# Performance work log

Hardware: AMD Instinct MI355X
Metric: run time of the kernel (lower is better)

Reference implementation:

```python
import jax, jax.numpy as jnp
import numpy as np

T = 8192   # sequence length (timesteps)
C = 1      # input channels
H = 51     # hidden size (module default)


def setup_inputs() -> dict:
    key = jax.random.key(0)
    ks = jax.random.split(key, 12)
    s = 1.0 / np.sqrt(H)  # PyTorch LSTMCell/Linear uniform init bound

    def u(k, shape):
        return jax.random.uniform(k, shape, jnp.float32, -s, s)

    return {
        "x": jax.random.normal(ks[0], (T, C), jnp.float32),
        # LSTMCell 1: input C -> hidden H
        "Wih1": u(ks[1], (4 * H, C)),
        "Whh1": u(ks[2], (4 * H, H)),
        "bih1": u(ks[3], (4 * H,)),
        "bhh1": u(ks[4], (4 * H,)),
        # LSTMCell 2: hidden H -> hidden H
        "Wih2": u(ks[5], (4 * H, H)),
        "Whh2": u(ks[6], (4 * H, H)),
        "bih2": u(ks[7], (4 * H,)),
        "bhh2": u(ks[8], (4 * H,)),
        # Output linear: H -> 1
        "Wlin": u(ks[9], (1, H)),
        "blin": u(ks[10], (1,)),
    }


def _lstm_cell(xt, h, c, Wih, Whh, bih, bhh):
    # PyTorch LSTMCell gate order: i, f, g, o
    z = xt @ Wih.T + h @ Whh.T + (bih + bhh)  # [1, 4H]
    i, f, g, o = jnp.split(z, 4, axis=-1)
    c_new = jax.nn.sigmoid(f) * c + jax.nn.sigmoid(i) * jnp.tanh(g)
    h_new = jax.nn.sigmoid(o) * jnp.tanh(c_new)
    return h_new, c_new


def reference(x, Wih1, Whh1, bih1, bhh1, Wih2, Whh2, bih2, bhh2, Wlin, blin):
    def step(carry, xt):
        h1, c1, h2, c2 = carry
        h1, c1 = _lstm_cell(xt, h1, c1, Wih1, Whh1, bih1, bhh1)
        h2, c2 = _lstm_cell(h1, h2, c2, Wih2, Whh2, bih2, bhh2)
        out = h2 @ Wlin.T + blin  # [1, 1]
        return (h1, c1, h2, c2), out[0]

    init = tuple(jnp.zeros((1, H), jnp.float32) for _ in range(4))
    _, outs = jax.lax.scan(step, init, x[:, None, :])  # per-step xt: [1, C]
    return outs  # [T, 1]
```

## Files before the change

kernel.cpp:

```cpp
#include <hip/hip_runtime.h>

#define TSTEPS 8192
#define H 51
#define SE 8
#define NEPOCH (TSTEPS / SE + 3)

typedef float  f2 __attribute__((ext_vector_type(2)));
typedef float  f4 __attribute__((ext_vector_type(4)));
typedef int    i4 __attribute__((ext_vector_type(4)));
typedef int    i2 __attribute__((ext_vector_type(2)));
typedef _Float16 h2 __attribute__((ext_vector_type(2)));

__device__ __forceinline__ int rl_i(int v, int k) { return __builtin_amdgcn_readlane(v, k); }
__device__ __forceinline__ h2 asp(int v) { union { int i; h2 h; } u; u.i = v; return u.h; }
__device__ __forceinline__ int ash(h2 v) { union { int i; h2 h; } u; u.h = v; return u.i; }

__device__ __forceinline__ float fdot2(h2 a, h2 b, float c) {
#if __has_builtin(__builtin_amdgcn_fdot2)
    return __builtin_amdgcn_fdot2(a, b, c, false);
#else
    return fmaf((float)a[0], (float)b[0], fmaf((float)a[1], (float)b[1], c));
#endif
}
__device__ __forceinline__ float sigmoidf_fast(float x) {
    return __builtin_amdgcn_rcpf(1.0f + __expf(-x));
}
__device__ __forceinline__ float tanhf_fast(float x) {
    x = fminf(fmaxf(x, -15.0f), 15.0f);
    float t = __expf(-2.0f * x);
    return (1.0f - t) * __builtin_amdgcn_rcpf(1.0f + t);
}
__device__ __forceinline__ int packpair(const float* Wrow, int j) {
    const float w0 = (2 * j < H) ? Wrow[2 * j] : 0.0f;
    const float w1 = (2 * j + 1 < H) ? Wrow[2 * j + 1] : 0.0f;
    h2 p; p[0] = (_Float16)w0; p[1] = (_Float16)w1; return ash(p);
}
__device__ __forceinline__ int packpairs_bperm(float hval, int a0, int a1) {
    const int hi = __float_as_int(hval);
    const float v0 = __int_as_float(__builtin_amdgcn_ds_bpermute(a0, hi));
    const float v1 = __int_as_float(__builtin_amdgcn_ds_bpermute(a1, hi));
    h2 pk; pk[0] = (_Float16)v0; pk[1] = (_Float16)v1;
    return ash(pk);
}

#define DECLG(g) i4 wq##g##_0, wq##g##_1, wq##g##_2, wq##g##_3, wq##g##_4, wq##g##_5; i2 wq##g##_6;
#define LOADG(g, RP) { const float* _r = (RP); \
    i4 t0 = {packpair(_r,0),  packpair(_r,1),  packpair(_r,2),  packpair(_r,3)};  wq##g##_0 = t0; \
    i4 t1 = {packpair(_r,4),  packpair(_r,5),  packpair(_r,6),  packpair(_r,7)};  wq##g##_1 = t1; \
    i4 t2 = {packpair(_r,8),  packpair(_r,9),  packpair(_r,10), packpair(_r,11)}; wq##g##_2 = t2; \
    i4 t3 = {packpair(_r,12), packpair(_r,13), packpair(_r,14), packpair(_r,15)}; wq##g##_3 = t3; \
    i4 t4 = {packpair(_r,16), packpair(_r,17), packpair(_r,18), packpair(_r,19)}; wq##g##_4 = t4; \
    i4 t5 = {packpair(_r,20), packpair(_r,21), packpair(_r,22), packpair(_r,23)}; wq##g##_5 = t5; \
    i2 t6 = {packpair(_r,24), packpair(_r,25)};                                   wq##g##_6 = t6; }
#define PING(g) asm("" : "+v"(wq##g##_0), "+v"(wq##g##_1), "+v"(wq##g##_2), \
                        "+v"(wq##g##_3), "+v"(wq##g##_4), "+v"(wq##g##_5), "+v"(wq##g##_6));
#define DJA(j,q,e) { const h2 _hb = asp(rl_i(_hs, j)); \
    a0 = fdot2(asp(wq0_##q[e]), _hb, a0); \
    a1 = fdot2(asp(wq1_##q[e]), _hb, a1); \
    a2 = fdot2(asp(wq2_##q[e]), _hb, a2); \
    a3 = fdot2(asp(wq3_##q[e]), _hb, a3); }
#define DJB(j,q,e) { const h2 _hb = asp(rl_i(_hs, j)); \
    b0 = fdot2(asp(wq0_##q[e]), _hb, b0); \
    b1 = fdot2(asp(wq1_##q[e]), _hb, b1); \
    b2 = fdot2(asp(wq2_##q[e]), _hb, b2); \
    b3 = fdot2(asp(wq3_##q[e]), _hb, b3); }
#define DOT26 \
    DJA(0,0,0) DJB(1,0,1) DJA(2,0,2) DJB(3,0,3) DJA(4,1,0) DJB(5,1,1) DJA(6,1,2) DJB(7,1,3) \
    DJA(8,2,0) DJB(9,2,1) DJA(10,2,2) DJB(11,2,3) DJA(12,3,0) DJB(13,3,1) DJA(14,3,2) DJB(15,3,3) \
    DJA(16,4,0) DJB(17,4,1) DJA(18,4,2) DJB(19,4,3) DJA(20,5,0) DJB(21,5,1) DJA(22,5,2) DJB(23,5,3) \
    DJA(24,6,0) DJB(25,6,1)

__global__ __launch_bounds__(256) __attribute__((amdgpu_waves_per_eu(1, 1)))
void lstm2_b8_kernel(const float* __restrict__ x,
                     const float* __restrict__ Wih1,
                     const float* __restrict__ Whh1,
                     const float* __restrict__ bih1,
                     const float* __restrict__ bhh1,
                     const float* __restrict__ Wih2,
                     const float* __restrict__ Whh2,
                     const float* __restrict__ bih2,
                     const float* __restrict__ bhh2,
                     const float* __restrict__ Wlin,
                     const float* __restrict__ blin,
                     float* __restrict__ out)
{
    __shared__ __align__(16) float sh_x[TSTEPS];
    __shared__ __align__(16) float sh_out[TSTEPS];
    __shared__ __align__(16) int   sh_hpk1[2][SE][64];
    __shared__ __align__(16) f4    sh_z2a[2][SE][64];
    __shared__ __align__(16) float sh_h2f[2][SE][64];

    const int tid  = threadIdx.x;
    const int wave = tid >> 6;
    const int lane = tid & 63;
    const int row  = (lane < H) ? lane : (H - 1);
    const int pa0  = (2 * lane) * 4;
    const int pa1  = (2 * lane + 1) * 4;

    for (int i = tid; i < TSTEPS / 4; i += 256)
        ((f4*)sh_x)[i] = ((const f4*)x)[i];

    const float* Mp = (wave == 0) ? Whh1 : (wave == 1) ? Whh2 : Wih2;
    DECLG(0) DECLG(1) DECLG(2) DECLG(3)
    LOADG(0, Mp + (0 * H + row) * H)
    LOADG(1, Mp + (1 * H + row) * H)
    LOADG(2, Mp + (2 * H + row) * H)
    LOADG(3, Mp + (3 * H + row) * H)
    PING(0) PING(1) PING(2) PING(3)

    f4 b1v, wx4, b2v;
#pragma unroll
    for (int g = 0; g < 4; ++g) {
        b1v[g] = bih1[g * H + row] + bhh1[g * H + row];
        wx4[g] = Wih1[g * H + row];
        b2v[g] = bih2[g * H + row] + bhh2[g * H + row];
    }
    const float wlin = (lane < H) ? Wlin[lane] : 0.0f;
    const float bl   = blin[0];

    if (tid < 64) {
#pragma unroll
        for (int b = 0; b < 2; ++b)
#pragma unroll
            for (int j = 0; j < SE; ++j) {
                sh_hpk1[b][j][tid] = 0;
                sh_z2a[b][j][tid] = (f4)0.0f;
                sh_h2f[b][j][tid] = 0.0f;
            }
    }
    float c1 = 0.0f, c2 = 0.0f;
    int hpk1reg = 0, hpk2reg = 0;
    __syncthreads();

#pragma unroll 1
    for (int e = 0; e < NEPOCH; ++e) {
        if (wave == 0) {
            if (e < TSTEPS / SE) {
                const f4 xs0 = ((const f4*)sh_x)[2 * e];
                const f4 xs1 = ((const f4*)sh_x)[2 * e + 1];
#pragma unroll
                for (int j = 0; j < SE; ++j) {
                    const float xv = (j < 4) ? xs0[j & 3] : xs1[j & 3];
                    float a0 = fmaf(wx4[0], xv, b1v[0]);
                    float a1 = fmaf(wx4[1], xv, b1v[1]);
                    float a2 = fmaf(wx4[2], xv, b1v[2]);
                    float a3 = fmaf(wx4[3], xv, b1v[3]);
                    float b0 = 0.0f, b1 = 0.0f, b2 = 0.0f, b3 = 0.0f;
                    const int _hs = hpk1reg;
                    DOT26
                    const float ig = sigmoidf_fast(a0 + b0), fg = sigmoidf_fast(a1 + b1);
                    const float gg = tanhf_fast(a2 + b2),    og = sigmoidf_fast(a3 + b3);
                    c1 = fmaf(fg, c1, ig * gg);
                    const float h1n = (lane < H) ? og * tanhf_fast(c1) : 0.0f;
                    hpk1reg = packpairs_bperm(h1n, pa0, pa1);
                    sh_hpk1[e & 1][j][lane] = hpk1reg;
                }
            }
        } else if (wave == 2) {
            if (e >= 1 && e <= TSTEPS / SE) {
                int hp[SE];
#pragma unroll
                for (int j = 0; j < SE; ++j) hp[j] = sh_hpk1[(e - 1) & 1][j][lane];
#pragma unroll
                for (int j = 0; j < SE; ++j) {
                    const int _hs = hp[j];
                    float a0 = 0.0f, a1 = 0.0f, a2 = 0.0f, a3 = 0.0f;
                    float b0 = 0.0f, b1 = 0.0f, b2 = 0.0f, b3 = 0.0f;
                    DOT26
                    f4 z; z[0] = a0 + b0; z[1] = a1 + b1; z[2] = a2 + b2; z[3] = a3 + b3;
                    sh_z2a[e & 1][j][lane] = z;
                }
            }
        } else if (wave == 1) {
            if (e >= 2 && e <= TSTEPS / SE + 1) {
                f4 za[SE];
#pragma unroll
                for (int j = 0; j < SE; ++j) za[j] = sh_z2a[(e - 1) & 1][j][lane];
#pragma unroll
                for (int j = 0; j < SE; ++j) {
                    float a0 = b2v[0], a1 = b2v[1], a2 = b2v[2], a3 = b2v[3];
                    float b0 = 0.0f, b1 = 0.0f, b2 = 0.0f, b3 = 0.0f;
                    const int _hs = hpk2reg;
                    DOT26
                    const float ig = sigmoidf_fast(za[j][0] + a0 + b0);
                    const float fg = sigmoidf_fast(za[j][1] + a1 + b1);
                    const float gg = tanhf_fast   (za[j][2] + a2 + b2);
                    const float og = sigmoidf_fast(za[j][3] + a3 + b3);
                    c2 = fmaf(fg, c2, ig * gg);
                    const float h2n = (lane < H) ? og * tanhf_fast(c2) : 0.0f;
                    sh_h2f[e & 1][j][lane] = h2n;
                    hpk2reg = packpairs_bperm(h2n, pa0, pa1);
                }
            }
        } else {
            if (e >= 3) {
                const int base = (e - 3) * SE;
                float p[SE];
#pragma unroll
                for (int j = 0; j < SE; ++j)
                    p[j] = sh_h2f[(e - 1) & 1][j][lane] * wlin;
#pragma unroll
                for (int off = 32; off >= 1; off >>= 1) {
#pragma unroll
                    for (int j = 0; j < SE; ++j) p[j] += __shfl_down(p[j], off);
                }
                if (lane == 0) {
#pragma unroll
                    for (int j = 0; j < SE; ++j) sh_out[base + j] = p[j] + bl;
                }
            }
        }
        __syncthreads();
    }

    for (int i = tid; i < TSTEPS / 4; i += 256)
        ((f4*)out)[i] = ((const f4*)sh_out)[i];
}

extern "C" void kernel_launch(void* const* d_in, const int* in_sizes, int n_in,
                              void* d_out, int out_size, void* d_ws, size_t ws_size,
                              hipStream_t stream) {
    const float* x    = (const float*)d_in[0];
    const float* Wih1 = (const float*)d_in[1];
    const float* Whh1 = (const float*)d_in[2];
    const float* bih1 = (const float*)d_in[3];
    const float* bhh1 = (const float*)d_in[4];
    const float* Wih2 = (const float*)d_in[5];
    const float* Whh2 = (const float*)d_in[6];
    const float* bih2 = (const float*)d_in[7];
    const float* bhh2 = (const float*)d_in[8];
    const float* Wlin = (const float*)d_in[9];
    const float* blin = (const float*)d_in[10];
    float* out = (float*)d_out;

    lstm2_b8_kernel<<<1, 256, 0, stream>>>(
        x, Wih1, Whh1, bih1, bhh1, Wih2, Whh2, bih2, bhh2, Wlin, blin, out);
}
```

Measured before the change: 3.223 ms.

## Fold log2e scaling into weights and reorder gate computation for latency

Pre-scales the gate weights and biases by log2(e) (2·log2(e) for the g gate), so the sigmoid and tanh activations can call exp2 directly without a multiply. Readlanes of the packed hidden state are hoisted into an array, and each gate's dot product is computed one gate at a time: g first, then f, i, o. This lets each transcendental start while the next gate's FMAs run, shortening the serial critical path of each recurrent step. The layer-2 z loads are split into two blocks of four to reduce register pressure. Prescaling the weights before fp16 packing changes rounding slightly, and the gate-activation tanh loses its clamp.

New measurement: 3.367 ms. 4.5% more time.

```diff
diff --git a/kernel.cpp b/kernel.cpp
--- a/kernel.cpp
+++ b/kernel.cpp
@@ -5,11 +5,12 @@
 #define SE 8
 #define NEPOCH (TSTEPS / SE + 3)
 
-typedef float  f2 __attribute__((ext_vector_type(2)));
 typedef float  f4 __attribute__((ext_vector_type(4)));
 typedef int    i4 __attribute__((ext_vector_type(4)));
 typedef int    i2 __attribute__((ext_vector_type(2)));
 typedef _Float16 h2 __attribute__((ext_vector_type(2)));
+
+#define LOG2E 1.44269504f
 
 __device__ __forceinline__ int rl_i(int v, int k) { return __builtin_amdgcn_readlane(v, k); }
 __device__ __forceinline__ h2 asp(int v) { union { int i; h2 h; } u; u.i = v; return u.h; }
@@ -22,17 +23,21 @@
     return fmaf((float)a[0], (float)b[0], fmaf((float)a[1], (float)b[1], c));
 #endif
 }
-__device__ __forceinline__ float sigmoidf_fast(float x) {
-    return __builtin_amdgcn_rcpf(1.0f + __expf(-x));
-}
-__device__ __forceinline__ float tanhf_fast(float x) {
+__device__ __forceinline__ float sig2(float x) {
+    return __builtin_amdgcn_rcpf(1.0f + exp2f(-x));
+}
+__device__ __forceinline__ float tanh2(float x) {
+    const float t = exp2f(-x);
+    return (1.0f - t) * __builtin_amdgcn_rcpf(1.0f + t);
+}
+__device__ __forceinline__ float tanh_c(float x) {
     x = fminf(fmaxf(x, -15.0f), 15.0f);
-    float t = __expf(-2.0f * x);
+    const float t = exp2f(-2.88539008f * x);
     return (1.0f - t) * __builtin_amdgcn_rcpf(1.0f + t);
 }
-__device__ __forceinline__ int packpair(const float* Wrow, int j) {
-    const float w0 = (2 * j < H) ? Wrow[2 * j] : 0.0f;
-    const float w1 = (2 * j + 1 < H) ? Wrow[2 * j + 1] : 0.0f;
+__device__ __forceinline__ int packpair(const float* Wrow, int j, float s) {
+    const float w0 = (2 * j < H) ? s * Wrow[2 * j] : 0.0f;
+    const float w1 = (2 * j + 1 < H) ? s * Wrow[2 * j + 1] : 0.0f;
     h2 p; p[0] = (_Float16)w0; p[1] = (_Float16)w1; return ash(p);
 }
 __device__ __forceinline__ int packpairs_bperm(float hval, int a0, int a1) {
@@ -44,45 +49,41 @@
 }
 
 #define DECLG(g) i4 wq##g##_0, wq##g##_1, wq##g##_2, wq##g##_3, wq##g##_4, wq##g##_5; i2 wq##g##_6;
-#define LOADG(g, RP) { const float* _r = (RP); \
-    i4 t0 = {packpair(_r,0),  packpair(_r,1),  packpair(_r,2),  packpair(_r,3)};  wq##g##_0 = t0; \
-    i4 t1 = {packpair(_r,4),  packpair(_r,5),  packpair(_r,6),  packpair(_r,7)};  wq##g##_1 = t1; \
-    i4 t2 = {packpair(_r,8),  packpair(_r,9),  packpair(_r,10), packpair(_r,11)}; wq##g##_2 = t2; \
-    i4 t3 = {packpair(_r,12), packpair(_r,13), packpair(_r,14), packpair(_r,15)}; wq##g##_3 = t3; \
-    i4 t4 = {packpair(_r,16), packpair(_r,17), packpair(_r,18), packpair(_r,19)}; wq##g##_4 = t4; \
-    i4 t5 = {packpair(_r,20), packpair(_r,21), packpair(_r,22), packpair(_r,23)}; wq##g##_5 = t5; \
-    i2 t6 = {packpair(_r,24), packpair(_r,25)};                                   wq##g##_6 = t6; }
+#define LOADG(g, RP, S) { const float* _r = (RP); const float _s = (S); \
+    i4 t0 = {packpair(_r,0,_s),  packpair(_r,1,_s),  packpair(_r,2,_s),  packpair(_r,3,_s)};  wq##g##_0 = t0; \
+    i4 t1 = {packpair(_r,4,_s),  packpair(_r,5,_s),  packpair(_r,6,_s),  packpair(_r,7,_s)};  wq##g##_1 = t1; \
+    i4 t2 = {packpair(_r,8,_s),  packpair(_r,9,_s),  packpair(_r,10,_s), packpair(_r,11,_s)}; wq##g##_2 = t2; \
+    i4 t3 = {packpair(_r,12,_s), packpair(_r,13,_s), packpair(_r,14,_s), packpair(_r,15,_s)}; wq##g##_3 = t3; \
+    i4 t4 = {packpair(_r,16,_s), packpair(_r,17,_s), packpair(_r,18,_s), packpair(_r,19,_s)}; wq##g##_4 = t4; \
+    i4 t5 = {packpair(_r,20,_s), packpair(_r,21,_s), packpair(_r,22,_s), packpair(_r,23,_s)}; wq##g##_5 = t5; \
+    i2 t6 = {packpair(_r,24,_s), packpair(_r,25,_s)};                                         wq##g##_6 = t6; }
 #define PING(g) asm("" : "+v"(wq##g##_0), "+v"(wq##g##_1), "+v"(wq##g##_2), \
                         "+v"(wq##g##_3), "+v"(wq##g##_4), "+v"(wq##g##_5), "+v"(wq##g##_6));
-#define DJA(j,q,e) { const h2 _hb = asp(rl_i(_hs, j)); \
-    a0 = fdot2(asp(wq0_##q[e]), _hb, a0); \
-    a1 = fdot2(asp(wq1_##q[e]), _hb, a1); \
-    a2 = fdot2(asp(wq2_##q[e]), _hb, a2); \
-    a3 = fdot2(asp(wq3_##q[e]), _hb, a3); }
-#define DJB(j,q,e) { const h2 _hb = asp(rl_i(_hs, j)); \
-    b0 = fdot2(asp(wq0_##q[e]), _hb, b0); \
-    b1 = fdot2(asp(wq1_##q[e]), _hb, b1); \
-    b2 = fdot2(asp(wq2_##q[e]), _hb, b2); \
-    b3 = fdot2(asp(wq3_##q[e]), _hb, b3); }
-#define DOT26 \
-    DJA(0,0,0) DJB(1,0,1) DJA(2,0,2) DJB(3,0,3) DJA(4,1,0) DJB(5,1,1) DJA(6,1,2) DJB(7,1,3) \
-    DJA(8,2,0) DJB(9,2,1) DJA(10,2,2) DJB(11,2,3) DJA(12,3,0) DJB(13,3,1) DJA(14,3,2) DJB(15,3,3) \
-    DJA(16,4,0) DJB(17,4,1) DJA(18,4,2) DJB(19,4,3) DJA(20,5,0) DJB(21,5,1) DJA(22,5,2) DJB(23,5,3) \
-    DJA(24,6,0) DJB(25,6,1)
+#define RL26(SRC) int hb[26]; { const int _h = (SRC); \
+    _Pragma("unroll") for (int _k = 0; _k < 26; ++_k) hb[_k] = rl_i(_h, _k); }
+#define DG(G,k,q,e,ACC) ACC = fdot2(asp(wq##G##_##q[e]), asp(hb[k]), ACC);
+#define DOTG(G,A,B) \
+    DG(G,0,0,0,A) DG(G,1,0,1,B) DG(G,2,0,2,A) DG(G,3,0,3,B) \
+    DG(G,4,1,0,A) DG(G,5,1,1,B) DG(G,6,1,2,A) DG(G,7,1,3,B) \
+    DG(G,8,2,0,A) DG(G,9,2,1,B) DG(G,10,2,2,A) DG(G,11,2,3,B) \
+    DG(G,12,3,0,A) DG(G,13,3,1,B) DG(G,14,3,2,A) DG(G,15,3,3,B) \
+    DG(G,16,4,0,A) DG(G,17,4,1,B) DG(G,18,4,2,A) DG(G,19,4,3,B) \
+    DG(G,20,5,0,A) DG(G,21,5,1,B) DG(G,22,5,2,A) DG(G,23,5,3,B) \
+    DG(G,24,6,0,A) DG(G,25,6,1,B)
 
 __global__ __launch_bounds__(256) __attribute__((amdgpu_waves_per_eu(1, 1)))
-void lstm2_b8_kernel(const float* __restrict__ x,
-                     const float* __restrict__ Wih1,
-                     const float* __restrict__ Whh1,
-                     const float* __restrict__ bih1,
-                     const float* __restrict__ bhh1,
-                     const float* __restrict__ Wih2,
-                     const float* __restrict__ Whh2,
-                     const float* __restrict__ bih2,
-                     const float* __restrict__ bhh2,
-                     const float* __restrict__ Wlin,
-                     const float* __restrict__ blin,
-                     float* __restrict__ out)
+void lstm2_lat_kernel(const float* __restrict__ x,
+                      const float* __restrict__ Wih1,
+                      const float* __restrict__ Whh1,
+                      const float* __restrict__ bih1,
+                      const float* __restrict__ bhh1,
+                      const float* __restrict__ Wih2,
+                      const float* __restrict__ Whh2,
+                      const float* __restrict__ bih2,
+                      const float* __restrict__ bhh2,
+                      const float* __restrict__ Wlin,
+                      const float* __restrict__ blin,
+                      float* __restrict__ out)
 {
     __shared__ __align__(16) float sh_x[TSTEPS];
     __shared__ __align__(16) float sh_out[TSTEPS];
@@ -100,20 +101,22 @@
     for (int i = tid; i < TSTEPS / 4; i += 256)
         ((f4*)sh_x)[i] = ((const f4*)x)[i];
 
+    const float scl[4] = {LOG2E, LOG2E, 2.0f * LOG2E, LOG2E};
+
     const float* Mp = (wave == 0) ? Whh1 : (wave == 1) ? Whh2 : Wih2;
     DECLG(0) DECLG(1) DECLG(2) DECLG(3)
-    LOADG(0, Mp + (0 * H + row) * H)
-    LOADG(1, Mp + (1 * H + row) * H)
-    LOADG(2, Mp + (2 * H + row) * H)
-    LOADG(3, Mp + (3 * H + row) * H)
+    LOADG(0, Mp + (0 * H + row) * H, scl[0])
+    LOADG(1, Mp + (1 * H + row) * H, scl[1])
+    LOADG(2, Mp + (2 * H + row) * H, scl[2])
+    LOADG(3, Mp + (3 * H + row) * H, scl[3])
     PING(0) PING(1) PING(2) PING(3)
 
     f4 b1v, wx4, b2v;
 #pragma unroll
     for (int g = 0; g < 4; ++g) {
-        b1v[g] = bih1[g * H + row] + bhh1[g * H + row];
-        wx4[g] = Wih1[g * H + row];
-        b2v[g] = bih2[g * H + row] + bhh2[g * H + row];
+        b1v[g] = scl[g] * (bih1[g * H + row] + bhh1[g * H + row]);
+        wx4[g] = scl[g] * Wih1[g * H + row];
+        b2v[g] = scl[g] * (bih2[g * H + row] + bhh2[g * H + row]);
     }
     const float wlin = (lane < H) ? Wlin[lane] : 0.0f;
     const float bl   = blin[0];
@@ -141,17 +144,22 @@
 #pragma unroll
                 for (int j = 0; j < SE; ++j) {
                     const float xv = (j < 4) ? xs0[j & 3] : xs1[j & 3];
-                    float a0 = fmaf(wx4[0], xv, b1v[0]);
-                    float a1 = fmaf(wx4[1], xv, b1v[1]);
-                    float a2 = fmaf(wx4[2], xv, b1v[2]);
-                    float a3 = fmaf(wx4[3], xv, b1v[3]);
-                    float b0 = 0.0f, b1 = 0.0f, b2 = 0.0f, b3 = 0.0f;
-                    const int _hs = hpk1reg;
-                    DOT26
-                    const float ig = sigmoidf_fast(a0 + b0), fg = sigmoidf_fast(a1 + b1);
-                    const float gg = tanhf_fast(a2 + b2),    og = sigmoidf_fast(a3 + b3);
-                    c1 = fmaf(fg, c1, ig * gg);
-                    const float h1n = (lane < H) ? og * tanhf_fast(c1) : 0.0f;
+                    RL26(hpk1reg)
+                    float g0 = fmaf(wx4[2], xv, b1v[2]), g1 = 0.0f;
+                    DOTG(2, g0, g1)
+                    const float tg = tanh2(g0 + g1);
+                    float f0 = fmaf(wx4[1], xv, b1v[1]), f1 = 0.0f;
+                    DOTG(1, f0, f1)
+                    const float sf = sig2(f0 + f1);
+                    float i0 = fmaf(wx4[0], xv, b1v[0]), i1 = 0.0f;
+                    DOTG(0, i0, i1)
+                    const float si = sig2(i0 + i1);
+                    c1 = fmaf(sf, c1, si * tg);
+                    float o0 = fmaf(wx4[3], xv, b1v[3]), o1 = 0.0f;
+                    DOTG(3, o0, o1)
+                    const float so = sig2(o0 + o1);
+                    const float tc = tanh_c(c1);
+                    const float h1n = (lane < H) ? so * tc : 0.0f;
                     hpk1reg = packpairs_bperm(h1n, pa0, pa1);
                     sh_hpk1[e & 1][j][lane] = hpk1reg;
                 }
@@ -163,33 +171,47 @@
                 for (int j = 0; j < SE; ++j) hp[j] = sh_hpk1[(e - 1) & 1][j][lane];
 #pragma unroll
                 for (int j = 0; j < SE; ++j) {
-                    const int _hs = hp[j];
-                    float a0 = 0.0f, a1 = 0.0f, a2 = 0.0f, a3 = 0.0f;
-                    float b0 = 0.0f, b1 = 0.0f, b2 = 0.0f, b3 = 0.0f;
-                    DOT26
-                    f4 z; z[0] = a0 + b0; z[1] = a1 + b1; z[2] = a2 + b2; z[3] = a3 + b3;
+                    RL26(hp[j])
+                    float a0 = 0.0f, a1 = 0.0f;
+                    DOTG(0, a0, a1)
+                    float bq0 = 0.0f, bq1 = 0.0f;
+                    DOTG(1, bq0, bq1)
+                    float cq0 = 0.0f, cq1 = 0.0f;
+                    DOTG(2, cq0, cq1)
+                    float dq0 = 0.0f, dq1 = 0.0f;
+                    DOTG(3, dq0, dq1)
+                    f4 z; z[0] = a0 + a1; z[1] = bq0 + bq1; z[2] = cq0 + cq1; z[3] = dq0 + dq1;
                     sh_z2a[e & 1][j][lane] = z;
                 }
             }
         } else if (wave == 1) {
             if (e >= 2 && e <= TSTEPS / SE + 1) {
-                f4 za[SE];
-#pragma unroll
-                for (int j = 0; j < SE; ++j) za[j] = sh_z2a[(e - 1) & 1][j][lane];
-#pragma unroll
-                for (int j = 0; j < SE; ++j) {
-                    float a0 = b2v[0], a1 = b2v[1], a2 = b2v[2], a3 = b2v[3];
-                    float b0 = 0.0f, b1 = 0.0f, b2 = 0.0f, b3 = 0.0f;
-                    const int _hs = hpk2reg;
-                    DOT26
-                    const float ig = sigmoidf_fast(za[j][0] + a0 + b0);
-                    const float fg = sigmoidf_fast(za[j][1] + a1 + b1);
-                    const float gg = tanhf_fast   (za[j][2] + a2 + b2);
-                    const float og = sigmoidf_fast(za[j][3] + a3 + b3);
-                    c2 = fmaf(fg, c2, ig * gg);
-                    const float h2n = (lane < H) ? og * tanhf_fast(c2) : 0.0f;
-                    sh_h2f[e & 1][j][lane] = h2n;
-                    hpk2reg = packpairs_bperm(h2n, pa0, pa1);
+#pragma unroll
+                for (int jb = 0; jb < 2; ++jb) {
+                    f4 za[4];
+#pragma unroll
+                    for (int j = 0; j < 4; ++j) za[j] = sh_z2a[(e - 1) & 1][jb * 4 + j][lane];
+#pragma unroll
+                    for (int j = 0; j < 4; ++j) {
+                        RL26(hpk2reg)
+                        float g0 = b2v[2] + za[j][2], g1 = 0.0f;
+                        DOTG(2, g0, g1)
+                        const float tg = tanh2(g0 + g1);
+                        float f0 = b2v[1] + za[j][1], f1 = 0.0f;
+                        DOTG(1, f0, f1)
+                        const float sf = sig2(f0 + f1);
+                        float i0 = b2v[0] + za[j][0], i1 = 0.0f;
+                        DOTG(0, i0, i1)
+                        const float si = sig2(i0 + i1);
+                        c2 = fmaf(sf, c2, si * tg);
+                        float o0 = b2v[3] + za[j][3], o1 = 0.0f;
+                        DOTG(3, o0, o1)
+                        const float so = sig2(o0 + o1);
+                        const float tc = tanh_c(c2);
+                        const float h2n = (lane < H) ? so * tc : 0.0f;
+                        sh_h2f[e & 1][jb * 4 + j][lane] = h2n;
+                        hpk2reg = packpairs_bperm(h2n, pa0, pa1);
+                    }
                 }
             }
         } else {
@@ -233,6 +255,6 @@
     const float* blin = (const float*)d_in[10];
     float* out = (float*)d_out;
 
-    lstm2_b8_kernel<<<1, 256, 0, stream>>>(
+    lstm2_lat_kernel<<<1, 256, 0, stream>>>(
         x, Wih1, Whh1, bih1, bhh1, Wih2, Whh2, bih2, bhh2, Wlin, blin, out);
 }
```
